# Kernel tuning notes

Measured on AMD Instinct MI355X. Metric: run time of the kernel, lower is better.

## Reference

```python
import jax, jax.numpy as jnp
import numpy as np

TEMPERATURE = 8.0  # sqrt(d_k)=sqrt(64)
NEG = -1000000000.0

def setup_inputs() -> dict:
    key = jax.random.key(0)
    kq, kk, kv, km = jax.random.split(key, 4)
    BH, S, D = 64, 1024, 64
    q = jax.random.normal(kq, (BH, S, D), dtype=jnp.float32)
    k = jax.random.normal(kk, (BH, S, D), dtype=jnp.float32)
    v = jax.random.normal(kv, (BH, S, D), dtype=jnp.float32)
    mask = jax.random.randint(km, (BH, 1, S), 0, 2).astype(jnp.int32)
    return {"q": q, "k": k, "v": v, "mask": mask}

def reference(q, k, v, mask):
    # attn scores: [BH, S, S]
    attn = jnp.einsum('bqd,bkd->bqk', q / TEMPERATURE, k)
    attn = jnp.where(mask == 0, NEG, attn)
    attn = jax.nn.softmax(attn, axis=-1)
    output = jnp.einsum('bqk,bkd->bqd', attn, v)
    return (output, attn)
```

## Files before the change

kernel.cpp:

```cpp
#include <hip/hip_runtime.h>
#include <stdint.h>

typedef unsigned short u16;
typedef u16 u16x8 __attribute__((ext_vector_type(8)));
typedef u16x8 __attribute__((may_alias)) u16x8a;
typedef float f32x4 __attribute__((ext_vector_type(4)));
typedef f32x4 __attribute__((may_alias)) f32x4a;
typedef __bf16 bf16x8 __attribute__((ext_vector_type(8)));
typedef float f32x16 __attribute__((ext_vector_type(16)));

#define S_LEN 1024
#define D_DIM 64
#define BHN   64

__device__ __forceinline__ bf16x8 cvt8(const float* p) {
  f32x4 a = *reinterpret_cast<const f32x4a*>(p);
  f32x4 b = *reinterpret_cast<const f32x4a*>(p + 4);
  bf16x8 r;
#pragma unroll
  for (int j = 0; j < 4; ++j) { r[j] = (__bf16)a[j]; r[4 + j] = (__bf16)b[j]; }
  return r;
}
__device__ __forceinline__ bf16x8 ldbf(const u16* p) {
  return __builtin_bit_cast(bf16x8, *reinterpret_cast<const u16x8a*>(p));
}

#define ORED_OFF   20480
#define RS_OFF     (ORED_OFF + 32 * 68 * 4)
#define INV_OFF    (RS_OFF + 512)
#define SMEM_BYTES (INV_OFF + 128)

__global__ __launch_bounds__(256, 3) void attn_kernel(
    const float* __restrict__ Q, const float* __restrict__ K, const int* __restrict__ Mk,
    const float* __restrict__ V, float* __restrict__ outO, float* __restrict__ outA) {
  __shared__ __align__(16) char smem[SMEM_BYTES];
  const int tid = threadIdx.x;
  const int wave = tid >> 6, lane = tid & 63;
  const int l31 = lane & 31, half = lane >> 5;

  const int id = blockIdx.x;
  const int xcd = id & 7, ord = id >> 3;
  const int bh = xcd * 8 + (ord >> 5);
  const int q0 = (ord & 31) << 5;

  u16* tbase = (u16*)smem;
  float* ored = (float*)(smem + ORED_OFF);
  float* rs_lds = (float*)(smem + RS_OFF);
  float* inv_lds = (float*)(smem + INV_OFF);

  for (int i = tid; i < 32 * 68; i += 256) ored[i] = 0.0f;

  const float* qb = Q + (((size_t)bh << 10) + q0 + l31) * D_DIM + half * 8;
  bf16x8 qa[4];
#pragma unroll
  for (int ks = 0; ks < 4; ++ks) qa[ks] = cvt8(qb + ks * 16);

  const int colbase = wave * 256;
  const float* kb0 = K + ((size_t)bh << 10) * D_DIM + half * 8;
  const int* mrow = Mk + ((size_t)bh << 10) + colbase + l31;

  bf16x8 pfrag[16];
  float rs[16];
#pragma unroll
  for (int r = 0; r < 16; ++r) rs[r] = 0.0f;

#pragma unroll
  for (int t = 0; t < 8; ++t) {
    u16* tile = tbase + (((t & 1) << 2) + wave) * (32 * 40);
    const float* kb = kb0 + (size_t)(colbase + t * 32 + l31) * D_DIM;
    f32x16 acc = 0.0f;
#pragma unroll
    for (int ks = 0; ks < 4; ++ks) {
      bf16x8 kf = cvt8(kb + ks * 16);
      acc = __builtin_amdgcn_mfma_f32_32x32x16_bf16(qa[ks], kf, acc, 0, 0, 0);
    }
    const float mf = (mrow[t * 32] == 0) ? 0.0f : 1.0f;
#pragma unroll
    for (int r = 0; r < 16; ++r) {
      float p = exp2f(acc[r] * 0.18033688f) * mf;
      __bf16 pb = (__bf16)p;
      rs[r] += (float)pb;
      const int row = (r & 3) + ((r >> 2) << 3) + (half << 2);
      tile[row * 40 + l31] = __builtin_bit_cast(u16, pb);
    }
    asm volatile("s_waitcnt lgkmcnt(0)" ::: "memory");
    __builtin_amdgcn_sched_barrier(0);
    pfrag[2 * t]     = ldbf(tile + l31 * 40 + half * 8);
    pfrag[2 * t + 1] = ldbf(tile + l31 * 40 + 16 + half * 8);
  }

#pragma unroll
  for (int r = 0; r < 16; ++r) {
    float s = rs[r];
#pragma unroll
    for (int m = 1; m < 32; m <<= 1) s += __shfl_xor(s, m, 64);
    rs[r] = s;
  }
  if (l31 == 0) {
#pragma unroll
    for (int r = 0; r < 16; ++r) {
      const int row = (r & 3) + ((r >> 2) << 3) + (half << 2);
      rs_lds[wave * 32 + row] = rs[r];
    }
  }
  __syncthreads();
  if (tid < 32) {
    float s = rs_lds[tid] + rs_lds[32 + tid] + rs_lds[64 + tid] + rs_lds[96 + tid];
    inv_lds[tid] = 1.0f / s;
  }
  __syncthreads();

  f32x16 oacc0 = 0.0f, oacc1 = 0.0f;
  const float* vb = V + (((size_t)bh << 10) + colbase + half * 8) * D_DIM + l31;
#pragma unroll
  for (int kk = 0; kk < 16; ++kk) {
    bf16x8 b0, b1;
#pragma unroll
    for (int jj = 0; jj < 8; ++jj) {
      b0[jj] = (__bf16)vb[(kk * 16 + jj) * D_DIM];
      b1[jj] = (__bf16)vb[(kk * 16 + jj) * D_DIM + 32];
    }
    oacc0 = __builtin_amdgcn_mfma_f32_32x32x16_bf16(pfrag[kk], b0, oacc0, 0, 0, 0);
    oacc1 = __builtin_amdgcn_mfma_f32_32x32x16_bf16(pfrag[kk], b1, oacc1, 0, 0, 0);
  }

  const float myinv = inv_lds[l31];
  float* ab = outA + ((size_t)bh << 20) + ((size_t)(q0 + l31) << 10) + colbase + half * 8;
#pragma unroll
  for (int t = 0; t < 8; ++t) {
#pragma unroll
    for (int f = 0; f < 2; ++f) {
      bf16x8 pf = pfrag[2 * t + f];
      f32x4 lo, hi;
#pragma unroll
      for (int j = 0; j < 4; ++j) {
        lo[j] = (float)pf[j] * myinv;
        hi[j] = (float)pf[4 + j] * myinv;
      }
      *reinterpret_cast<f32x4a*>(ab + t * 32 + f * 16) = lo;
      *reinterpret_cast<f32x4a*>(ab + t * 32 + f * 16 + 4) = hi;
    }
  }

#pragma unroll
  for (int r = 0; r < 16; ++r) {
    const int row = (r & 3) + ((r >> 2) << 3) + (half << 2);
    atomicAdd(&ored[row * 68 + l31], oacc0[r]);
    atomicAdd(&ored[row * 68 + 32 + l31], oacc1[r]);
  }
  asm volatile("s_waitcnt lgkmcnt(0)" ::: "memory");
  __builtin_amdgcn_s_barrier();
  __builtin_amdgcn_sched_barrier(0);

  const int orow = tid >> 3;
  const int oc = (tid & 7) * 8;
  const float iv = inv_lds[orow];
  f32x4 o0 = *reinterpret_cast<const f32x4a*>(ored + orow * 68 + oc);
  f32x4 o1 = *reinterpret_cast<const f32x4a*>(ored + orow * 68 + oc + 4);
#pragma unroll
  for (int jj = 0; jj < 4; ++jj) { o0[jj] *= iv; o1[jj] *= iv; }
  float* ob = outO + (((size_t)bh << 10) + q0 + orow) * D_DIM + oc;
  *reinterpret_cast<f32x4a*>(ob) = o0;
  *reinterpret_cast<f32x4a*>(ob + 4) = o1;
}

extern "C" void kernel_launch(void* const* d_in, const int* in_sizes, int n_in,
                              void* d_out, int out_size, void* d_ws, size_t ws_size,
                              hipStream_t stream) {
  (void)in_sizes; (void)n_in; (void)out_size; (void)d_ws; (void)ws_size;
  const float* Q = (const float*)d_in[0];
  const float* K = (const float*)d_in[1];
  const float* V = (const float*)d_in[2];
  const int*   M = (const int*)d_in[3];
  float* outO = (float*)d_out;
  float* outA = outO + (size_t)BHN * S_LEN * D_DIM;

  attn_kernel<<<dim3(BHN * (S_LEN / 32)), dim3(256), 0, stream>>>(Q, K, M, V, outO, outA);
}
```

Before: 469.6 us.

## Compute transposed scores to build P fragments in registers, dropping LDS transpose

Swaps the MFMA operand order so each lane holds a row of the score tile directly in the A-fragment layout. P fragments can then be packed in registers instead of round-tripping through an LDS tile. The mask is precomputed once per block into an LDS additive bias in the permuted column order. Row sums collapse to one shuffle, and V loads are software-prefetched one step ahead. The permuted K-index layout changes V row indexing and the attn store offsets, and the extra prefetch registers add register pressure.

```diff
diff --git a/kernel.cpp b/kernel.cpp
--- a/kernel.cpp
+++ b/kernel.cpp
@@ -2,17 +2,20 @@
 #include <stdint.h>
 
 typedef unsigned short u16;
-typedef u16 u16x8 __attribute__((ext_vector_type(8)));
-typedef u16x8 __attribute__((may_alias)) u16x8a;
+typedef unsigned u32;
 typedef float f32x4 __attribute__((ext_vector_type(4)));
 typedef f32x4 __attribute__((may_alias)) f32x4a;
 typedef __bf16 bf16x8 __attribute__((ext_vector_type(8)));
+typedef u32 u32x4 __attribute__((ext_vector_type(4)));
 typedef float f32x16 __attribute__((ext_vector_type(16)));
 
 #define S_LEN 1024
 #define D_DIM 64
 #define BHN   64
 
+__device__ __forceinline__ float bf2f(u16 b) {
+  return __builtin_bit_cast(float, (u32)b << 16);
+}
 __device__ __forceinline__ bf16x8 cvt8(const float* p) {
   f32x4 a = *reinterpret_cast<const f32x4a*>(p);
   f32x4 b = *reinterpret_cast<const f32x4a*>(p + 4);
@@ -21,11 +24,9 @@
   for (int j = 0; j < 4; ++j) { r[j] = (__bf16)a[j]; r[4 + j] = (__bf16)b[j]; }
   return r;
 }
-__device__ __forceinline__ bf16x8 ldbf(const u16* p) {
-  return __builtin_bit_cast(bf16x8, *reinterpret_cast<const u16x8a*>(p));
-}
 
-#define ORED_OFF   20480
+#define MB_OFF     0
+#define ORED_OFF   4096
 #define RS_OFF     (ORED_OFF + 32 * 68 * 4)
 #define INV_OFF    (RS_OFF + 512)
 #define SMEM_BYTES (INV_OFF + 128)
@@ -43,11 +44,18 @@
   const int bh = xcd * 8 + (ord >> 5);
   const int q0 = (ord & 31) << 5;
 
-  u16* tbase = (u16*)smem;
+  float* mbias = (float*)(smem + MB_OFF);
   float* ored = (float*)(smem + ORED_OFF);
   float* rs_lds = (float*)(smem + RS_OFF);
   float* inv_lds = (float*)(smem + INV_OFF);
 
+  const int* maskp = Mk + ((size_t)bh << 10);
+  for (int i = tid; i < 1024; i += 256) {
+    const int w = i >> 8, rem = i & 255;
+    const int t = rem >> 5, hi = (rem >> 4) & 1, r = rem & 15;
+    const int col = (w << 8) + (t << 5) + (r & 3) + ((r >> 2) << 3) + (hi << 2);
+    mbias[i] = (maskp[col] == 0) ? -1.0e9f : 0.0f;
+  }
   for (int i = tid; i < 32 * 68; i += 256) ored[i] = 0.0f;
 
   const float* qb = Q + (((size_t)bh << 10) + q0 + l31) * D_DIM + half * 8;
@@ -55,54 +63,43 @@
 #pragma unroll
   for (int ks = 0; ks < 4; ++ks) qa[ks] = cvt8(qb + ks * 16);
 
+  __syncthreads();
+
   const int colbase = wave * 256;
   const float* kb0 = K + ((size_t)bh << 10) * D_DIM + half * 8;
-  const int* mrow = Mk + ((size_t)bh << 10) + colbase + l31;
+  const float* mbw = mbias + (wave << 8) + (half << 4);
 
   bf16x8 pfrag[16];
-  float rs[16];
-#pragma unroll
-  for (int r = 0; r < 16; ++r) rs[r] = 0.0f;
+  float rs = 0.0f;
 
 #pragma unroll
   for (int t = 0; t < 8; ++t) {
-    u16* tile = tbase + (((t & 1) << 2) + wave) * (32 * 40);
     const float* kb = kb0 + (size_t)(colbase + t * 32 + l31) * D_DIM;
     f32x16 acc = 0.0f;
 #pragma unroll
     for (int ks = 0; ks < 4; ++ks) {
       bf16x8 kf = cvt8(kb + ks * 16);
-      acc = __builtin_amdgcn_mfma_f32_32x32x16_bf16(qa[ks], kf, acc, 0, 0, 0);
+      acc = __builtin_amdgcn_mfma_f32_32x32x16_bf16(kf, qa[ks], acc, 0, 0, 0);
     }
-    const float mf = (mrow[t * 32] == 0) ? 0.0f : 1.0f;
+    const float* mb = mbw + (t << 5);
+    u32 w[8];
 #pragma unroll
-    for (int r = 0; r < 16; ++r) {
-      float p = exp2f(acc[r] * 0.18033688f) * mf;
-      __bf16 pb = (__bf16)p;
-      rs[r] += (float)pb;
-      const int row = (r & 3) + ((r >> 2) << 3) + (half << 2);
-      tile[row * 40 + l31] = __builtin_bit_cast(u16, pb);
+    for (int i = 0; i < 8; ++i) {
+      const float p0 = exp2f((acc[2 * i] + mb[2 * i]) * 0.18033688f);
+      const float p1 = exp2f((acc[2 * i + 1] + mb[2 * i + 1]) * 0.18033688f);
+      const u16 b0 = __builtin_bit_cast(u16, (__bf16)p0);
+      const u16 b1 = __builtin_bit_cast(u16, (__bf16)p1);
+      rs += bf2f(b0) + bf2f(b1);
+      w[i] = ((u32)b1 << 16) | (u32)b0;
     }
-    asm volatile("s_waitcnt lgkmcnt(0)" ::: "memory");
-    __builtin_amdgcn_sched_barrier(0);
-    pfrag[2 * t]     = ldbf(tile + l31 * 40 + half * 8);
-    pfrag[2 * t + 1] = ldbf(tile + l31 * 40 + 16 + half * 8);
+    u32x4 f0 = {w[0], w[1], w[2], w[3]};
+    u32x4 f1 = {w[4], w[5], w[6], w[7]};
+    pfrag[2 * t] = __builtin_bit_cast(bf16x8, f0);
+    pfrag[2 * t + 1] = __builtin_bit_cast(bf16x8, f1);
   }
 
-#pragma unroll
-  for (int r = 0; r < 16; ++r) {
-    float s = rs[r];
-#pragma unroll
-    for (int m = 1; m < 32; m <<= 1) s += __shfl_xor(s, m, 64);
-    rs[r] = s;
-  }
-  if (l31 == 0) {
-#pragma unroll
-    for (int r = 0; r < 16; ++r) {
-      const int row = (r & 3) + ((r >> 2) << 3) + (half << 2);
-      rs_lds[wave * 32 + row] = rs[r];
-    }
-  }
+  const float rsw = rs + __shfl_xor(rs, 32, 64);
+  if (half == 0) rs_lds[(wave << 5) + l31] = rsw;
   __syncthreads();
   if (tid < 32) {
     float s = rs_lds[tid] + rs_lds[32 + tid] + rs_lds[64 + tid] + rs_lds[96 + tid];
@@ -111,21 +108,37 @@
   __syncthreads();
 
   f32x16 oacc0 = 0.0f, oacc1 = 0.0f;
-  const float* vb = V + (((size_t)bh << 10) + colbase + half * 8) * D_DIM + l31;
+  const float* vb = V + (((size_t)bh << 10) + colbase + half * 4) * D_DIM + l31;
+  float cv0[8], cv1[8];
+#pragma unroll
+  for (int jj = 0; jj < 8; ++jj) {
+    const int vo = ((jj & 3) + 8 * (jj >> 2)) * D_DIM;
+    cv0[jj] = vb[vo]; cv1[jj] = vb[vo + 32];
+  }
 #pragma unroll
   for (int kk = 0; kk < 16; ++kk) {
+    float nv0[8], nv1[8];
+    if (kk < 15) {
+      const float* vn = vb + (size_t)(kk + 1) * 16 * D_DIM;
+#pragma unroll
+      for (int jj = 0; jj < 8; ++jj) {
+        const int vo = ((jj & 3) + 8 * (jj >> 2)) * D_DIM;
+        nv0[jj] = vn[vo]; nv1[jj] = vn[vo + 32];
+      }
+    }
     bf16x8 b0, b1;
 #pragma unroll
-    for (int jj = 0; jj < 8; ++jj) {
-      b0[jj] = (__bf16)vb[(kk * 16 + jj) * D_DIM];
-      b1[jj] = (__bf16)vb[(kk * 16 + jj) * D_DIM + 32];
-    }
+    for (int jj = 0; jj < 8; ++jj) { b0[jj] = (__bf16)cv0[jj]; b1[jj] = (__bf16)cv1[jj]; }
     oacc0 = __builtin_amdgcn_mfma_f32_32x32x16_bf16(pfrag[kk], b0, oacc0, 0, 0, 0);
     oacc1 = __builtin_amdgcn_mfma_f32_32x32x16_bf16(pfrag[kk], b1, oacc1, 0, 0, 0);
+    if (kk < 15) {
+#pragma unroll
+      for (int jj = 0; jj < 8; ++jj) { cv0[jj] = nv0[jj]; cv1[jj] = nv1[jj]; }
+    }
   }
 
   const float myinv = inv_lds[l31];
-  float* ab = outA + ((size_t)bh << 20) + ((size_t)(q0 + l31) << 10) + colbase + half * 8;
+  float* ab = outA + ((size_t)bh << 20) + ((size_t)(q0 + l31) << 10) + colbase + half * 4;
 #pragma unroll
   for (int t = 0; t < 8; ++t) {
 #pragma unroll
@@ -138,7 +151,7 @@
         hi[j] = (float)pf[4 + j] * myinv;
       }
       *reinterpret_cast<f32x4a*>(ab + t * 32 + f * 16) = lo;
-      *reinterpret_cast<f32x4a*>(ab + t * 32 + f * 16 + 4) = hi;
+      *reinterpret_cast<f32x4a*>(ab + t * 32 + f * 16 + 8) = hi;
     }
   }
 
```

Measured after the change: 675.6 us. +43.9%, slower.
